# Kernel tuning notes

Measured on AMD Instinct MI355X. Metric: run time of the kernel, lower is better.

## Reference

```python
import jax, jax.numpy as jnp
import numpy as np

N, IN, H, C = 50000, 128, 4, 32
E = 800000
NEG_SLOPE = 0.2


def setup_inputs() -> dict:
    key = jax.random.key(0)
    ks = jax.random.split(key, 8)
    x = jax.random.normal(ks[0], (N, IN), dtype=jnp.float32)
    edge_index = jax.random.randint(ks[1], (2, E), 0, N, dtype=jnp.int64)
    s = 0.1
    W = jax.random.normal(ks[2], (H * C, IN), dtype=jnp.float32) * s
    att_src = jax.random.normal(ks[3], (1, H, C), dtype=jnp.float32) * s
    att_dst = jax.random.normal(ks[4], (1, H, C), dtype=jnp.float32) * s
    bias = jnp.zeros((H * C,), dtype=jnp.float32)
    skip_W = jax.random.normal(ks[5], (H * C, IN), dtype=jnp.float32) * s
    skip_b = jnp.zeros((H * C,), dtype=jnp.float32)
    return {"x": x, "edge_index": edge_index, "W": W, "att_src": att_src,
            "att_dst": att_dst, "bias": bias, "skip_W": skip_W, "skip_b": skip_b}


def reference(x, edge_index, W, att_src, att_dst, bias, skip_W, skip_b):
    src, dst = edge_index[0], edge_index[1]
    # projected node features: [N, H, C]
    xp = (x @ W.T).reshape(N, H, C)
    # per-node attention logits: [N, H]
    a_src = jnp.sum(xp * att_src, axis=-1)
    a_dst = jnp.sum(xp * att_dst, axis=-1)
    # edge logits with LeakyReLU: [E, H]
    e = a_src[src] + a_dst[dst]
    e = jnp.where(e > 0, e, NEG_SLOPE * e)
    # segment softmax over incoming edges of each dst node
    m = jax.ops.segment_max(e, dst, num_segments=N)  # [N, H]
    ex = jnp.exp(e - m[dst])
    denom = jax.ops.segment_sum(ex, dst, num_segments=N)  # [N, H]
    alpha = ex / (denom[dst] + 1e-16)
    # weighted messages and scatter-add aggregation: [N, H, C]
    msg = alpha[:, :, None] * xp[src]
    agg = jax.ops.segment_sum(msg, dst, num_segments=N)
    x_gat = agg.reshape(N, H * C) + bias
    x_skip = x @ skip_W.T + skip_b
    return jax.nn.elu(x_gat + x_skip)
```

## Files before the change

### kernel.cpp

```cpp
#include <hip/hip_runtime.h>
#include <hip/hip_bf16.h>


#define NN 50000
#define EE 800000
#define FD 128
#define NEG_SLOPE 0.2f

#define SCB 1024
#define NB_SC ((NN + SCB - 1) / SCB)
#define NB_HIST (EE / 256)
#define NB_CONVW 32
#define NB_MFMA (NN / 16)

typedef __attribute__((ext_vector_type(8))) short short8;
typedef __attribute__((ext_vector_type(4))) float f32x4;

__device__ inline ushort f2b(float f) {
    __hip_bfloat16 h = __float2bfloat16(f);
    return *reinterpret_cast<ushort*>(&h);
}
__device__ inline float b2f(ushort u) {
    union { float f; unsigned int i; } c;
    c.i = ((unsigned int)u) << 16;
    return c.f;
}

__global__ __launch_bounds__(256) void gat_pre_kernel(
    const int* __restrict__ idx, int* __restrict__ count, int* __restrict__ rank,
    const float* __restrict__ W, const float* __restrict__ skip_W,
    ushort* __restrict__ wb)
{
    int b = blockIdx.x;
    if (b < NB_HIST) {
        int k = b * 256 + threadIdx.x;
        int d = idx[EE + k];
        rank[k] = atomicAdd(&count[d], 1);
    } else {
        int i = ((b - NB_HIST) * 256 + threadIdx.x) * 4;
        int row = i >> 7;
        int colb = i & 127;
        const float* src = (row < 128) ? (W + row * FD + colb)
                                       : (skip_W + (row - 128) * FD + colb);
        float4 v = *reinterpret_cast<const float4*>(src);
        ushort4 o;
        o.x = f2b(v.x); o.y = f2b(v.y); o.z = f2b(v.z); o.w = f2b(v.w);
        *reinterpret_cast<ushort4*>(wb + i) = o;
    }
}

__global__ __launch_bounds__(1024) void gat_blocksum_kernel(
    const int* __restrict__ count, int* __restrict__ bsum)
{
    __shared__ int ws[16];
    int tid = threadIdx.x, lane = tid & 63, wv = tid >> 6;
    int i = blockIdx.x * SCB + tid;
    int v = (i < NN) ? count[i] : 0;
    #pragma unroll
    for (int off = 32; off; off >>= 1) v += __shfl_down(v, off, 64);
    if (lane == 0) ws[wv] = v;
    __syncthreads();
    if (wv == 0) {
        int t = (lane < 16) ? ws[lane] : 0;
        #pragma unroll
        for (int off = 8; off; off >>= 1) t += __shfl_down(t, off, 64);
        if (lane == 0) bsum[blockIdx.x] = t;
    }
}

__global__ __launch_bounds__(1024) void gat_scan_kernel(
    const int* __restrict__ count, const int* __restrict__ bsum,
    int* __restrict__ rowptr)
{
    __shared__ int ws[16];
    __shared__ int boff_s;
    int tid = threadIdx.x, lane = tid & 63, wv = tid >> 6;
    int i = blockIdx.x * SCB + tid;
    int v = (i < NN) ? count[i] : 0;
    int incl = v;
    #pragma unroll
    for (int off = 1; off < 64; off <<= 1) {
        int t = __shfl_up(incl, off, 64);
        if (lane >= off) incl += t;
    }
    if (lane == 63) ws[wv] = incl;
    __syncthreads();
    if (wv == 0) {
        int t = (lane < 16) ? ws[lane] : 0;
        int winc = t;
        #pragma unroll
        for (int off = 1; off < 16; off <<= 1) {
            int u = __shfl_up(winc, off, 64);
            if (lane >= off) winc += u;
        }
        if (lane < 16) ws[lane] = winc - t;
    } else if (wv == 1) {
        int t = (lane < blockIdx.x) ? bsum[lane] : 0;
        #pragma unroll
        for (int off = 32; off; off >>= 1) t += __shfl_down(t, off, 64);
        if (lane == 0) boff_s = t;
    }
    __syncthreads();
    int excl = boff_s + ws[wv] + incl - v;
    if (i < NN) rowptr[i] = excl;
    if (blockIdx.x == 0 && tid == 0) rowptr[NN] = EE;
}

__global__ __launch_bounds__(256) void gat_mfma_fill_kernel(
    const float* __restrict__ x, const ushort* __restrict__ wb,
    const float* __restrict__ att_src, const float* __restrict__ att_dst,
    const float* __restrict__ bias, const float* __restrict__ skip_b,
    ushort* __restrict__ xpb, float* __restrict__ a_src, float* __restrict__ a_dst,
    float* __restrict__ skip,
    const int* __restrict__ idx, const int* __restrict__ rank,
    const int* __restrict__ rowptr, int* __restrict__ col)
{
    if (blockIdx.x >= NB_MFMA) {
        int k = (blockIdx.x - NB_MFMA) * 256 + threadIdx.x;
        int d = idx[EE + k];
        col[rowptr[d] + rank[k]] = idx[k];
        return;
    }

    const int tid = threadIdx.x;
    const int w = tid >> 6;
    const int l = tid & 63;
    const int lrow = l & 15;
    const int lgrp = l >> 4;
    const int m0 = blockIdx.x * 16;
    const int is_skip = w >> 1;
    const int ncb = (w & 1) * 64;

    short8 bfrag[4][4];
    const ushort* wbase = wb + (size_t)(is_skip * 128 + ncb) * FD;
    #pragma unroll
    for (int t = 0; t < 4; ++t)
        #pragma unroll
        for (int kk = 0; kk < 4; ++kk)
            bfrag[t][kk] = *reinterpret_cast<const short8*>(
                wbase + (size_t)(t * 16 + lrow) * FD + kk * 32 + lgrp * 8);

    short8 afrag[4];
    const float* xrow = x + (size_t)(m0 + lrow) * FD + lgrp * 8;
    #pragma unroll
    for (int kk = 0; kk < 4; ++kk) {
        float4 a0 = *reinterpret_cast<const float4*>(xrow + kk * 32);
        float4 a1 = *reinterpret_cast<const float4*>(xrow + kk * 32 + 4);
        short8 af;
        af[0] = f2b(a0.x); af[1] = f2b(a0.y); af[2] = f2b(a0.z); af[3] = f2b(a0.w);
        af[4] = f2b(a1.x); af[5] = f2b(a1.y); af[6] = f2b(a1.z); af[7] = f2b(a1.w);
        afrag[kk] = af;
    }

    f32x4 acc[4];
    #pragma unroll
    for (int t = 0; t < 4; ++t) acc[t] = (f32x4){0.f, 0.f, 0.f, 0.f};

    #pragma unroll
    for (int kk = 0; kk < 4; ++kk)
        #pragma unroll
        for (int t = 0; t < 4; ++t)
            acc[t] = __builtin_amdgcn_mfma_f32_16x16x32_bf16(
                afrag[kk], bfrag[t][kk], acc[t], 0, 0, 0);

    if (is_skip) {
        #pragma unroll
        for (int t = 0; t < 4; ++t) {
            int colt = ncb + t * 16 + lrow;
            float add = skip_b[colt] + bias[colt];
            #pragma unroll
            for (int r = 0; r < 4; ++r) {
                int row = m0 + lgrp * 4 + r;
                skip[(size_t)row * FD + colt] = acc[t][r] + add;
            }
        }
    } else {
        float as[4], ad[4];
        #pragma unroll
        for (int t = 0; t < 4; ++t) {
            int colt = ncb + t * 16 + lrow;
            as[t] = att_src[colt];
            ad[t] = att_dst[colt];
            #pragma unroll
            for (int r = 0; r < 4; ++r) {
                int row = m0 + lgrp * 4 + r;
                xpb[(size_t)row * FD + colt] = f2b(acc[t][r]);
            }
        }
        const int h0 = ncb >> 5;
        #pragma unroll
        for (int r = 0; r < 4; ++r) {
            float p0 = acc[0][r] * as[0] + acc[1][r] * as[1];
            float p1 = acc[2][r] * as[2] + acc[3][r] * as[3];
            float q0 = acc[0][r] * ad[0] + acc[1][r] * ad[1];
            float q1 = acc[2][r] * ad[2] + acc[3][r] * ad[3];
            #pragma unroll
            for (int m = 1; m < 16; m <<= 1) {
                p0 += __shfl_xor(p0, m, 64);
                p1 += __shfl_xor(p1, m, 64);
                q0 += __shfl_xor(q0, m, 64);
                q1 += __shfl_xor(q1, m, 64);
            }
            if (lrow == 0) {
                int row = m0 + lgrp * 4 + r;
                a_src[(size_t)row * 4 + h0]     = p0;
                a_src[(size_t)row * 4 + h0 + 1] = p1;
                a_dst[(size_t)row * 4 + h0]     = q0;
                a_dst[(size_t)row * 4 + h0 + 1] = q1;
            }
        }
    }
}

__global__ __launch_bounds__(256) void gat_gather_kernel(
    const int* __restrict__ rowptr, const int* __restrict__ col,
    const float* __restrict__ a_src, const float* __restrict__ a_dst,
    const ushort* __restrict__ xpb, const float* __restrict__ skip,
    float* __restrict__ out)
{
    int wid = (blockIdx.x * 256 + threadIdx.x) >> 6;
    const int d = __builtin_amdgcn_readfirstlane(wid);
    int lane = threadIdx.x & 63;
    const int h = lane >> 4;
    const int ch = lane * 2;
    const float ad = a_dst[(size_t)d * 4 + h];
    const int beg = rowptr[d], end = rowptr[d + 1];
    float2 sk = *reinterpret_cast<const float2*>(skip + (size_t)d * FD + ch);

    float accx = 0.f, accy = 0.f, asum = 0.f;
    int j = beg;
    for (; j + 4 <= end; j += 4) {
        int s0 = col[j], s1 = col[j + 1], s2 = col[j + 2], s3 = col[j + 3];
        float e0 = a_src[(size_t)s0 * 4 + h] + ad;
        float e1 = a_src[(size_t)s1 * 4 + h] + ad;
        float e2 = a_src[(size_t)s2 * 4 + h] + ad;
        float e3 = a_src[(size_t)s3 * 4 + h] + ad;
        ushort2 x0 = *reinterpret_cast<const ushort2*>(xpb + (size_t)s0 * FD + ch);
        ushort2 x1 = *reinterpret_cast<const ushort2*>(xpb + (size_t)s1 * FD + ch);
        ushort2 x2 = *reinterpret_cast<const ushort2*>(xpb + (size_t)s2 * FD + ch);
        ushort2 x3 = *reinterpret_cast<const ushort2*>(xpb + (size_t)s3 * FD + ch);
        e0 = e0 > 0.f ? e0 : NEG_SLOPE * e0;
        e1 = e1 > 0.f ? e1 : NEG_SLOPE * e1;
        e2 = e2 > 0.f ? e2 : NEG_SLOPE * e2;
        e3 = e3 > 0.f ? e3 : NEG_SLOPE * e3;
        float p0 = __expf(e0), p1 = __expf(e1), p2 = __expf(e2), p3 = __expf(e3);
        asum += (p0 + p1) + (p2 + p3);
        accx += p0 * b2f(x0.x) + p1 * b2f(x1.x) + p2 * b2f(x2.x) + p3 * b2f(x3.x);
        accy += p0 * b2f(x0.y) + p1 * b2f(x1.y) + p2 * b2f(x2.y) + p3 * b2f(x3.y);
    }
    for (; j < end; ++j) {
        int s = col[j];
        float e = a_src[(size_t)s * 4 + h] + ad;
        ushort2 xv = *reinterpret_cast<const ushort2*>(xpb + (size_t)s * FD + ch);
        e = e > 0.f ? e : NEG_SLOPE * e;
        float p = __expf(e);
        asum += p;
        accx += p * b2f(xv.x);
        accy += p * b2f(xv.y);
    }
    float inv = 1.f / (asum + 1e-16f);
    float r0 = sk.x + accx * inv;
    float r1 = sk.y + accy * inv;
    r0 = r0 > 0.f ? r0 : expm1f(r0);
    r1 = r1 > 0.f ? r1 : expm1f(r1);
    *reinterpret_cast<float2*>(out + (size_t)d * FD + ch) = make_float2(r0, r1);
}

extern "C" void kernel_launch(void* const* d_in, const int* in_sizes, int n_in,
                              void* d_out, int out_size, void* d_ws, size_t ws_size,
                              hipStream_t stream)
{
    const float* x       = (const float*)d_in[0];
    const int*   idx     = (const int*)d_in[1];
    const float* W       = (const float*)d_in[2];
    const float* att_src = (const float*)d_in[3];
    const float* att_dst = (const float*)d_in[4];
    const float* bias    = (const float*)d_in[5];
    const float* skip_W  = (const float*)d_in[6];
    const float* skip_b  = (const float*)d_in[7];
    float*       out     = (float*)d_out;

    float*  ws     = (float*)d_ws;
    float*  skip   = ws;
    float*  a_src  = ws + 6400000;
    float*  a_dst  = ws + 6600000;
    int*    count  = (int*)(ws + 6800000);
    int*    rowptr = (int*)(ws + 6852000);
    int*    col    = (int*)(ws + 6956000);
    int*    rank   = (int*)(ws + 7756000);
    int*    bsum   = (int*)(ws + 8556000);
    ushort* xpb    = (ushort*)(ws + 8600000);
    ushort* wb     = (ushort*)(ws + 11900000);

    hipMemsetAsync(count, 0, (size_t)NN * sizeof(int), stream);

    gat_pre_kernel<<<NB_HIST + NB_CONVW, 256, 0, stream>>>(idx, count, rank, W, skip_W, wb);

    gat_blocksum_kernel<<<NB_SC, SCB, 0, stream>>>(count, bsum);
    gat_scan_kernel<<<NB_SC, SCB, 0, stream>>>(count, bsum, rowptr);

    gat_mfma_fill_kernel<<<NB_MFMA + NB_HIST, 256, 0, stream>>>(
        x, wb, att_src, att_dst, bias, skip_b, xpb, a_src, a_dst, skip,
        idx, rank, rowptr, col);

    gat_gather_kernel<<<(NN * 64) / 256, 256, 0, stream>>>(
        rowptr, col, a_src, a_dst, xpb, skip, out);
}
```

Before: 135.0 us.

## Pack a_src with bf16 features per row, merge scan kernels, interleave fused blocks

Stores the per-node source attention logits inside each padded bf16 feature row, so the gather kernel reads logits and features from one row rather than two arrays. The gather loop is unrolled to 8 edges so more loads are in flight. The histogram pass now handles four edges per thread with int4 loads. The two-kernel block-sum/scan is merged into one kernel that recomputes prefix sums redundantly, saving a launch. Fused MFMA and fill blocks are interleaved with a modular permutation and the col scatter uses nontemporal stores. The costs are the row padding and the redundant prefix reads in the scan.

```diff
diff --git a/kernel.cpp b/kernel.cpp
--- a/kernel.cpp
+++ b/kernel.cpp
@@ -7,11 +7,14 @@
 #define FD 128
 #define NEG_SLOPE 0.2f
 
+#define ROWU 136
 #define SCB 1024
 #define NB_SC ((NN + SCB - 1) / SCB)
-#define NB_HIST (EE / 256)
+#define NB_PRE 782
 #define NB_CONVW 32
 #define NB_MFMA (NN / 16)
+#define NB_FILL (EE / 256)
+#define NB_FUSED (NB_MFMA + NB_FILL)
 
 typedef __attribute__((ext_vector_type(8))) short short8;
 typedef __attribute__((ext_vector_type(4))) float f32x4;
@@ -32,12 +35,18 @@
     ushort* __restrict__ wb)
 {
     int b = blockIdx.x;
-    if (b < NB_HIST) {
-        int k = b * 256 + threadIdx.x;
-        int d = idx[EE + k];
-        rank[k] = atomicAdd(&count[d], 1);
+    if (b < NB_PRE) {
+        int base = (b * 256 + threadIdx.x) * 4;
+        if (base >= EE) return;
+        int4 dd = *reinterpret_cast<const int4*>(idx + EE + base);
+        int4 rr;
+        rr.x = atomicAdd(&count[dd.x], 1);
+        rr.y = atomicAdd(&count[dd.y], 1);
+        rr.z = atomicAdd(&count[dd.z], 1);
+        rr.w = atomicAdd(&count[dd.w], 1);
+        *reinterpret_cast<int4*>(rank + base) = rr;
     } else {
-        int i = ((b - NB_HIST) * 256 + threadIdx.x) * 4;
+        int i = ((b - NB_PRE) * 256 + threadIdx.x) * 4;
         int row = i >> 7;
         int colb = i & 127;
         const float* src = (row < 128) ? (W + row * FD + colb)
@@ -49,32 +58,27 @@
     }
 }
 
-__global__ __launch_bounds__(1024) void gat_blocksum_kernel(
-    const int* __restrict__ count, int* __restrict__ bsum)
+__global__ __launch_bounds__(1024) void gat_scan_kernel(
+    const int* __restrict__ count, int* __restrict__ rowptr)
 {
     __shared__ int ws[16];
+    __shared__ int boff_s;
     int tid = threadIdx.x, lane = tid & 63, wv = tid >> 6;
-    int i = blockIdx.x * SCB + tid;
-    int v = (i < NN) ? count[i] : 0;
-    #pragma unroll
-    for (int off = 32; off; off >>= 1) v += __shfl_down(v, off, 64);
-    if (lane == 0) ws[wv] = v;
+
+    int ps = 0;
+    for (int i = tid; i < blockIdx.x * SCB; i += SCB) ps += count[i];
+    #pragma unroll
+    for (int off = 32; off; off >>= 1) ps += __shfl_down(ps, off, 64);
+    if (lane == 0) ws[wv] = ps;
     __syncthreads();
     if (wv == 0) {
         int t = (lane < 16) ? ws[lane] : 0;
         #pragma unroll
         for (int off = 8; off; off >>= 1) t += __shfl_down(t, off, 64);
-        if (lane == 0) bsum[blockIdx.x] = t;
-    }
-}
-
-__global__ __launch_bounds__(1024) void gat_scan_kernel(
-    const int* __restrict__ count, const int* __restrict__ bsum,
-    int* __restrict__ rowptr)
-{
-    __shared__ int ws[16];
-    __shared__ int boff_s;
-    int tid = threadIdx.x, lane = tid & 63, wv = tid >> 6;
+        if (lane == 0) boff_s = t;
+    }
+    __syncthreads();
+
     int i = blockIdx.x * SCB + tid;
     int v = (i < NN) ? count[i] : 0;
     int incl = v;
@@ -94,11 +98,6 @@
             if (lane >= off) winc += u;
         }
         if (lane < 16) ws[lane] = winc - t;
-    } else if (wv == 1) {
-        int t = (lane < blockIdx.x) ? bsum[lane] : 0;
-        #pragma unroll
-        for (int off = 32; off; off >>= 1) t += __shfl_down(t, off, 64);
-        if (lane == 0) boff_s = t;
     }
     __syncthreads();
     int excl = boff_s + ws[wv] + incl - v;
@@ -110,15 +109,16 @@
     const float* __restrict__ x, const ushort* __restrict__ wb,
     const float* __restrict__ att_src, const float* __restrict__ att_dst,
     const float* __restrict__ bias, const float* __restrict__ skip_b,
-    ushort* __restrict__ xpb, float* __restrict__ a_src, float* __restrict__ a_dst,
-    float* __restrict__ skip,
+    ushort* __restrict__ xpr, float* __restrict__ a_dst, float* __restrict__ skip,
     const int* __restrict__ idx, const int* __restrict__ rank,
     const int* __restrict__ rowptr, int* __restrict__ col)
 {
-    if (blockIdx.x >= NB_MFMA) {
-        int k = (blockIdx.x - NB_MFMA) * 256 + threadIdx.x;
+    const int p = (int)(((long long)blockIdx.x * 2501) % NB_FUSED);
+    if (p >= NB_MFMA) {
+        int k = (p - NB_MFMA) * 256 + threadIdx.x;
         int d = idx[EE + k];
-        col[rowptr[d] + rank[k]] = idx[k];
+        int pos = rowptr[d] + rank[k];
+        __builtin_nontemporal_store(idx[k], &col[pos]);
         return;
     }
 
@@ -127,7 +127,7 @@
     const int l = tid & 63;
     const int lrow = l & 15;
     const int lgrp = l >> 4;
-    const int m0 = blockIdx.x * 16;
+    const int m0 = p * 16;
     const int is_skip = w >> 1;
     const int ncb = (w & 1) * 64;
 
@@ -184,7 +184,7 @@
             #pragma unroll
             for (int r = 0; r < 4; ++r) {
                 int row = m0 + lgrp * 4 + r;
-                xpb[(size_t)row * FD + colt] = f2b(acc[t][r]);
+                xpr[(size_t)row * ROWU + 8 + colt] = f2b(acc[t][r]);
             }
         }
         const int h0 = ncb >> 5;
@@ -203,8 +203,9 @@
             }
             if (lrow == 0) {
                 int row = m0 + lgrp * 4 + r;
-                a_src[(size_t)row * 4 + h0]     = p0;
-                a_src[(size_t)row * 4 + h0 + 1] = p1;
+                float* arow = reinterpret_cast<float*>(xpr + (size_t)row * ROWU);
+                arow[h0]     = p0;
+                arow[h0 + 1] = p1;
                 a_dst[(size_t)row * 4 + h0]     = q0;
                 a_dst[(size_t)row * 4 + h0 + 1] = q1;
             }
@@ -214,9 +215,8 @@
 
 __global__ __launch_bounds__(256) void gat_gather_kernel(
     const int* __restrict__ rowptr, const int* __restrict__ col,
-    const float* __restrict__ a_src, const float* __restrict__ a_dst,
-    const ushort* __restrict__ xpb, const float* __restrict__ skip,
-    float* __restrict__ out)
+    const float* __restrict__ a_dst, const ushort* __restrict__ xpr,
+    const float* __restrict__ skip, float* __restrict__ out)
 {
     int wid = (blockIdx.x * 256 + threadIdx.x) >> 6;
     const int d = __builtin_amdgcn_readfirstlane(wid);
@@ -229,34 +229,38 @@
 
     float accx = 0.f, accy = 0.f, asum = 0.f;
     int j = beg;
-    for (; j + 4 <= end; j += 4) {
-        int s0 = col[j], s1 = col[j + 1], s2 = col[j + 2], s3 = col[j + 3];
-        float e0 = a_src[(size_t)s0 * 4 + h] + ad;
-        float e1 = a_src[(size_t)s1 * 4 + h] + ad;
-        float e2 = a_src[(size_t)s2 * 4 + h] + ad;
-        float e3 = a_src[(size_t)s3 * 4 + h] + ad;
-        ushort2 x0 = *reinterpret_cast<const ushort2*>(xpb + (size_t)s0 * FD + ch);
-        ushort2 x1 = *reinterpret_cast<const ushort2*>(xpb + (size_t)s1 * FD + ch);
-        ushort2 x2 = *reinterpret_cast<const ushort2*>(xpb + (size_t)s2 * FD + ch);
-        ushort2 x3 = *reinterpret_cast<const ushort2*>(xpb + (size_t)s3 * FD + ch);
-        e0 = e0 > 0.f ? e0 : NEG_SLOPE * e0;
-        e1 = e1 > 0.f ? e1 : NEG_SLOPE * e1;
-        e2 = e2 > 0.f ? e2 : NEG_SLOPE * e2;
-        e3 = e3 > 0.f ? e3 : NEG_SLOPE * e3;
-        float p0 = __expf(e0), p1 = __expf(e1), p2 = __expf(e2), p3 = __expf(e3);
-        asum += (p0 + p1) + (p2 + p3);
-        accx += p0 * b2f(x0.x) + p1 * b2f(x1.x) + p2 * b2f(x2.x) + p3 * b2f(x3.x);
-        accy += p0 * b2f(x0.y) + p1 * b2f(x1.y) + p2 * b2f(x2.y) + p3 * b2f(x3.y);
+    for (; j + 8 <= end; j += 8) {
+        int s[8];
+        float e[8];
+        ushort2 xv[8];
+        #pragma unroll
+        for (int i = 0; i < 8; ++i) s[i] = col[j + i];
+        #pragma unroll
+        for (int i = 0; i < 8; ++i) {
+            const ushort* row = xpr + (size_t)s[i] * ROWU;
+            e[i] = reinterpret_cast<const float*>(row)[h] + ad;
+            xv[i] = *reinterpret_cast<const ushort2*>(row + 8 + ch);
+        }
+        #pragma unroll
+        for (int i = 0; i < 8; ++i) {
+            float ei = e[i];
+            ei = ei > 0.f ? ei : NEG_SLOPE * ei;
+            float pi = __expf(ei);
+            asum += pi;
+            accx += pi * b2f(xv[i].x);
+            accy += pi * b2f(xv[i].y);
+        }
     }
     for (; j < end; ++j) {
         int s = col[j];
-        float e = a_src[(size_t)s * 4 + h] + ad;
-        ushort2 xv = *reinterpret_cast<const ushort2*>(xpb + (size_t)s * FD + ch);
+        const ushort* row = xpr + (size_t)s * ROWU;
+        float e = reinterpret_cast<const float*>(row)[h] + ad;
+        ushort2 xv = *reinterpret_cast<const ushort2*>(row + 8 + ch);
         e = e > 0.f ? e : NEG_SLOPE * e;
-        float p = __expf(e);
-        asum += p;
-        accx += p * b2f(xv.x);
-        accy += p * b2f(xv.y);
+        float pe = __expf(e);
+        asum += pe;
+        accx += pe * b2f(xv.x);
+        accy += pe * b2f(xv.y);
     }
     float inv = 1.f / (asum + 1e-16f);
     float r0 = sk.x + accx * inv;
@@ -282,27 +286,24 @@
 
     float*  ws     = (float*)d_ws;
     float*  skip   = ws;
-    float*  a_src  = ws + 6400000;
-    float*  a_dst  = ws + 6600000;
-    int*    count  = (int*)(ws + 6800000);
-    int*    rowptr = (int*)(ws + 6852000);
-    int*    col    = (int*)(ws + 6956000);
-    int*    rank   = (int*)(ws + 7756000);
-    int*    bsum   = (int*)(ws + 8556000);
-    ushort* xpb    = (ushort*)(ws + 8600000);
+    float*  a_dst  = ws + 6400000;
+    int*    count  = (int*)(ws + 6600000);
+    int*    rowptr = (int*)(ws + 6652000);
+    int*    col    = (int*)(ws + 6756000);
+    int*    rank   = (int*)(ws + 7556000);
+    ushort* xpr    = (ushort*)(ws + 8400000);
     ushort* wb     = (ushort*)(ws + 11900000);
 
     hipMemsetAsync(count, 0, (size_t)NN * sizeof(int), stream);
 
-    gat_pre_kernel<<<NB_HIST + NB_CONVW, 256, 0, stream>>>(idx, count, rank, W, skip_W, wb);
-
-    gat_blocksum_kernel<<<NB_SC, SCB, 0, stream>>>(count, bsum);
-    gat_scan_kernel<<<NB_SC, SCB, 0, stream>>>(count, bsum, rowptr);
-
-    gat_mfma_fill_kernel<<<NB_MFMA + NB_HIST, 256, 0, stream>>>(
-        x, wb, att_src, att_dst, bias, skip_b, xpb, a_src, a_dst, skip,
+    gat_pre_kernel<<<NB_PRE + NB_CONVW, 256, 0, stream>>>(idx, count, rank, W, skip_W, wb);
+
+    gat_scan_kernel<<<NB_SC, SCB, 0, stream>>>(count, rowptr);
+
+    gat_mfma_fill_kernel<<<NB_FUSED, 256, 0, stream>>>(
+        x, wb, att_src, att_dst, bias, skip_b, xpr, a_dst, skip,
         idx, rank, rowptr, col);
 
     gat_gather_kernel<<<(NN * 64) / 256, 256, 0, stream>>>(
-        rowptr, col, a_src, a_dst, xpb, skip, out);
-}
+        rowptr, col, a_dst, xpr, skip, out);
+}
```

Measured after the change: 147.7 us. 9.4% more time.
